# Kernel tuning notes

Measured on AMD Instinct MI355X. Metric: run time of the kernel, lower is better.

## Reference

```python
import jax, jax.numpy as jnp
import numpy as np

B, L, DM = 4, 4096, 1024
DK, DV = 128, 128


def setup_inputs() -> dict:
    key = jax.random.key(0)
    kq, kk, kv, kwq, kwk, kwv = jax.random.split(key, 6)
    scale = 1.0 / np.sqrt(DM)
    return {
        "Q": jax.random.normal(kq, (B, L, DM), dtype=jnp.float32),
        "K": jax.random.normal(kk, (B, L, DM), dtype=jnp.float32),
        "V": jax.random.normal(kv, (B, L, DM), dtype=jnp.float32),
        "mask": jnp.ones((B, 1, L), dtype=jnp.int32),
        "WQ": jax.random.normal(kwq, (DM, DK), dtype=jnp.float32) * scale,
        "WK": jax.random.normal(kwk, (DM, DK), dtype=jnp.float32) * scale,
        "WV": jax.random.normal(kwv, (DM, DV), dtype=jnp.float32) * scale,
    }


def reference(Q, K, V, mask, WQ, WK, WV):
    # Projections (Dense, no bias): [B, L, dm] @ [dm, dk/dv]
    q = jnp.einsum("bld,dk->blk", Q, WQ)  # [B, L, dk]
    k = jnp.einsum("bld,dk->blk", K, WK)  # [B, L, dk]
    v = jnp.einsum("bld,dv->blv", V, WV)  # [B, L, dv]
    # Raw scores [B, L, L]
    qk = jnp.einsum("bqk,bsk->bqs", q, k)
    # Faithful to original: mask applied BEFORE scaling by 1/sqrt(dk)
    qk = jnp.where(mask == 1, qk, -jnp.inf)
    qk = qk / jnp.sqrt(jnp.asarray(DK, dtype=qk.dtype))
    attn = jax.nn.softmax(qk, axis=-1)
    return jnp.einsum("bqs,bsv->bqv", attn, v)  # [B, L, dv]
```

## Files before the change

### kernel.cpp

```cpp
#include <hip/hip_runtime.h>
#include <hip/hip_bf16.h>

#define B_  4
#define L_  4096
#define DM_ 1024
#define DK_ 128
#define DV_ 128
#define KS_ 4
#define ROWS_ (B_ * L_)

typedef __bf16 bf16x8 __attribute__((ext_vector_type(8)));
typedef float  f32x4  __attribute__((ext_vector_type(4)));

__device__ __forceinline__ float wred_max16(float v) {
    v = fmaxf(v, __shfl_xor(v, 1, 64));
    v = fmaxf(v, __shfl_xor(v, 2, 64));
    v = fmaxf(v, __shfl_xor(v, 4, 64));
    v = fmaxf(v, __shfl_xor(v, 8, 64));
    return v;
}
__device__ __forceinline__ float wred_sum16(float v) {
    v += __shfl_xor(v, 1, 64);
    v += __shfl_xor(v, 2, 64);
    v += __shfl_xor(v, 4, 64);
    v += __shfl_xor(v, 8, 64);
    return v;
}

__global__ __launch_bounds__(256) void wt_kernel(
    const float* __restrict__ WQ, const float* __restrict__ WK,
    const float* __restrict__ WV, __bf16* __restrict__ WT)
{
    const int mat = blockIdx.y;
    const float* W = (mat == 0) ? WQ : (mat == 1) ? WK : WV;
    __bf16* Wt = WT + (size_t)mat * DK_ * DM_;

    __shared__ float lds[DK_][33];
    const int t  = threadIdx.x;
    const int d0 = blockIdx.x * 32;

    for (int i = 0; i < 16; ++i) {
        int idx = i * 256 + t;
        int dd = idx >> 7, n = idx & 127;
        lds[n][dd] = W[(size_t)(d0 + dd) * DK_ + n];
    }
    __syncthreads();
    for (int i = 0; i < 16; ++i) {
        int idx = i * 256 + t;
        int n = idx >> 5, dd = idx & 31;
        Wt[(size_t)n * DM_ + d0 + dd] = (__bf16)lds[n][dd];
    }
}

__global__ __launch_bounds__(256) void proj_kernel(
    const float* __restrict__ Q, const float* __restrict__ K, const float* __restrict__ V,
    const __bf16* __restrict__ WT,
    __bf16* __restrict__ qb, __bf16* __restrict__ kb, __bf16* __restrict__ vT)
{
    const int mat = blockIdx.y;
    const float* X = (mat == 0) ? Q : (mat == 1) ? K : V;
    const __bf16* Wt = WT + (size_t)mat * DK_ * DM_;

    __shared__ __bf16 w_lds[128][132];

    const int t    = threadIdx.x;
    const int w    = t >> 6;
    const int l    = t & 63;
    const int quad = l >> 4;
    const int c16  = l & 15;
    const int m0   = blockIdx.x * 64 + w * 16;
    const float* xrow = &X[(size_t)(m0 + c16) * DM_];

    f32x4 acc[8];
    for (int i = 0; i < 8; ++i) acc[i] = {0.f, 0.f, 0.f, 0.f};

    for (int kt8 = 0; kt8 < 8; ++kt8) {
        const int d0 = kt8 * 128;
        __syncthreads();
        for (int i = 0; i < 8; ++i) {
            int e = i * 256 + t;
            int n = e >> 4, blk = e & 15;
            *(int4*)&w_lds[n][blk * 8] = *(const int4*)&Wt[(size_t)n * DM_ + d0 + blk * 8];
        }
        __syncthreads();

        for (int dd = 0; dd < 4; ++dd) {
            const float* xp = xrow + d0 + dd * 32 + quad * 8;
            float4 x0 = *(const float4*)xp;
            float4 x1 = *(const float4*)(xp + 4);
            bf16x8 af;
            af[0] = (__bf16)x0.x; af[1] = (__bf16)x0.y; af[2] = (__bf16)x0.z; af[3] = (__bf16)x0.w;
            af[4] = (__bf16)x1.x; af[5] = (__bf16)x1.y; af[6] = (__bf16)x1.z; af[7] = (__bf16)x1.w;
            for (int nt = 0; nt < 8; ++nt) {
                bf16x8 bfv = *(const bf16x8*)&w_lds[nt * 16 + c16][dd * 32 + quad * 8];
                acc[nt] = __builtin_amdgcn_mfma_f32_16x16x32_bf16(af, bfv, acc[nt], 0, 0, 0);
            }
        }
    }

    if (mat < 2) {
        __bf16* outp = (mat == 0) ? qb : kb;
        for (int nt = 0; nt < 8; ++nt)
            for (int r = 0; r < 4; ++r)
                outp[(size_t)(m0 + quad * 4 + r) * DK_ + nt * 16 + c16] = (__bf16)acc[nt][r];
    } else {
        for (int nt = 0; nt < 8; ++nt)
            for (int r = 0; r < 4; ++r) {
                int row = m0 + quad * 4 + r;
                int b = row >> 12, s = row & (L_ - 1);
                vT[((size_t)b * DV_ + nt * 16 + c16) * L_ + s] = (__bf16)acc[nt][r];
            }
    }
}

__global__ __launch_bounds__(256) void attn_kernel(
    const __bf16* __restrict__ qb, const __bf16* __restrict__ kb,
    const __bf16* __restrict__ vT, const int* __restrict__ mask,
    __bf16* __restrict__ ob_part, float* __restrict__ ml_part)
{
    __shared__ __bf16 k_lds[64][140];
    __shared__ __bf16 v_lds[128][76];
    __shared__ __bf16 p_lds[4][16][76];

    const int t    = threadIdx.x;
    const int w    = t >> 6;
    const int l    = t & 63;
    const int quad = l >> 4;
    const int c16  = l & 15;

    const int combo = blockIdx.x & 15;
    const int b     = combo & 3;
    const int ks    = combo >> 2;
    const int qt    = blockIdx.x >> 4;
    const int m0    = qt * 64 + w * 16;
    const size_t bL = (size_t)b * L_;
    const int kbase = ks * (L_ / KS_);

    bf16x8 qf[4];
    {
        const __bf16* qrow = &qb[(bL + m0 + c16) * DK_];
        for (int dt = 0; dt < 4; ++dt)
            qf[dt] = *(const bf16x8*)&qrow[dt * 32 + quad * 8];
    }

    f32x4 o[8];
    for (int i = 0; i < 8; ++i) o[i] = {0.f, 0.f, 0.f, 0.f};
    float mst[4], lst[4];
    for (int r = 0; r < 4; ++r) { mst[r] = -1e30f; lst[r] = 0.f; }

    const float sm_scale = 0.088388347648318447f;

    for (int sc = 0; sc < (L_ / KS_) / 64; ++sc) {
        const int s0 = kbase + sc * 64;
        __syncthreads();
        for (int i = 0; i < 4; ++i) {
            int e = i * 256 + t;
            int kr = e >> 4, c8 = (e & 15) << 3;
            *(int4*)&k_lds[kr][c8] = *(const int4*)&kb[(bL + s0 + kr) * DK_ + c8];
        }
        for (int i = 0; i < 4; ++i) {
            int e = i * 256 + t;
            int vr = e >> 3, s8 = (e & 7) << 3;
            *(int4*)&v_lds[vr][s8] = *(const int4*)&vT[((size_t)b * DV_ + vr) * L_ + s0 + s8];
        }
        __syncthreads();

        f32x4 sacc[4];
        for (int nt = 0; nt < 4; ++nt) sacc[nt] = {0.f, 0.f, 0.f, 0.f};
        for (int dt = 0; dt < 4; ++dt)
            for (int nt = 0; nt < 4; ++nt) {
                bf16x8 kf = *(const bf16x8*)&k_lds[nt * 16 + c16][dt * 32 + quad * 8];
                sacc[nt] = __builtin_amdgcn_mfma_f32_16x16x32_bf16(qf[dt], kf, sacc[nt], 0, 0, 0);
            }

        int mk[4];
        for (int nt = 0; nt < 4; ++nt) mk[nt] = mask[bL + s0 + nt * 16 + c16];
        for (int nt = 0; nt < 4; ++nt)
            for (int r = 0; r < 4; ++r) {
                float s = sacc[nt][r] * sm_scale;
                sacc[nt][r] = (mk[nt] == 1) ? s : -1e30f;
            }

        float alpha[4];
        for (int r = 0; r < 4; ++r) {
            float cm = fmaxf(fmaxf(sacc[0][r], sacc[1][r]), fmaxf(sacc[2][r], sacc[3][r]));
            cm = wred_max16(cm);
            float nm = fmaxf(mst[r], cm);
            alpha[r] = __expf(mst[r] - nm);
            float psum = 0.f;
            for (int nt = 0; nt < 4; ++nt) {
                float p = __expf(sacc[nt][r] - nm);
                __bf16 pbv = (__bf16)p;
                p_lds[w][quad * 4 + r][nt * 16 + c16] = pbv;
                psum += (float)pbv;
            }
            psum = wred_sum16(psum);
            lst[r] = lst[r] * alpha[r] + psum;
            mst[r] = nm;
        }
        __asm__ volatile("s_waitcnt lgkmcnt(0)" ::: "memory");

        for (int vt = 0; vt < 8; ++vt)
            for (int r = 0; r < 4; ++r)
                o[vt][r] *= alpha[r];

        for (int kt = 0; kt < 2; ++kt) {
            bf16x8 pf = *(const bf16x8*)&p_lds[w][c16][kt * 32 + quad * 8];
            for (int vt = 0; vt < 8; ++vt) {
                bf16x8 vf = *(const bf16x8*)&v_lds[vt * 16 + c16][kt * 32 + quad * 8];
                o[vt] = __builtin_amdgcn_mfma_f32_16x16x32_bf16(pf, vf, o[vt], 0, 0, 0);
            }
        }
    }

    __bf16* op = ob_part + ((size_t)ks * ROWS_ + bL + m0) * DV_;
    for (int vt = 0; vt < 8; ++vt)
        for (int r = 0; r < 4; ++r)
            op[(size_t)(quad * 4 + r) * DV_ + vt * 16 + c16] = (__bf16)o[vt][r];
    if (c16 == 0)
        for (int r = 0; r < 4; ++r) {
            size_t row = (size_t)ks * ROWS_ + bL + m0 + quad * 4 + r;
            ml_part[row * 2 + 0] = mst[r];
            ml_part[row * 2 + 1] = lst[r];
        }
}

__global__ __launch_bounds__(256) void combine_kernel(
    const __bf16* __restrict__ ob_part, const float* __restrict__ ml_part,
    float* __restrict__ out)
{
    const int gid = blockIdx.x * 256 + threadIdx.x;
    const int row = gid >> 5;
    const int c4  = (gid & 31) << 2;

    float m[KS_], lv[KS_];
    float M = -1e30f;
    for (int s = 0; s < KS_; ++s) {
        m[s]  = ml_part[((size_t)s * ROWS_ + row) * 2 + 0];
        lv[s] = ml_part[((size_t)s * ROWS_ + row) * 2 + 1];
        M = fmaxf(M, m[s]);
    }
    float Lt = 0.f, acc[4] = {0.f, 0.f, 0.f, 0.f};
    for (int s = 0; s < KS_; ++s) {
        float ws = __expf(m[s] - M);
        Lt += lv[s] * ws;
        const __bf16* op = ob_part + ((size_t)s * ROWS_ + row) * DV_ + c4;
        for (int c = 0; c < 4; ++c) acc[c] += (float)op[c] * ws;
    }
    float rL = 1.0f / Lt;
    for (int c = 0; c < 4; ++c)
        out[(size_t)row * DV_ + c4 + c] = acc[c] * rL;
}

extern "C" void kernel_launch(void* const* d_in, const int* in_sizes, int n_in,
                              void* d_out, int out_size, void* d_ws, size_t ws_size,
                              hipStream_t stream) {
    const float* Q    = (const float*)d_in[0];
    const float* K    = (const float*)d_in[1];
    const float* V    = (const float*)d_in[2];
    const int*   mask = (const int*)d_in[3];
    const float* WQ   = (const float*)d_in[4];
    const float* WK   = (const float*)d_in[5];
    const float* WV   = (const float*)d_in[6];
    float* out = (float*)d_out;

    __bf16* qb = (__bf16*)d_ws;
    __bf16* kb = qb + (size_t)ROWS_ * DK_;
    __bf16* vT = kb + (size_t)ROWS_ * DK_;
    __bf16* WT = vT + (size_t)ROWS_ * DV_;
    __bf16* ob_part = WT + (size_t)3 * DK_ * DM_;
    float*  ml_part = (float*)(ob_part + (size_t)KS_ * ROWS_ * DV_);

    wt_kernel<<<dim3(DM_ / 32, 3), 256, 0, stream>>>(WQ, WK, WV, WT);
    proj_kernel<<<dim3(ROWS_ / 64, 3), 256, 0, stream>>>(Q, K, V, WT, qb, kb, vT);
    attn_kernel<<<dim3((ROWS_ / 64) * KS_), 256, 0, stream>>>(qb, kb, vT, mask, ob_part, ml_part);
    combine_kernel<<<dim3(ROWS_ * 32 / 256), 256, 0, stream>>>(ob_part, ml_part, out);
}
```

Before: 335.0 us.

## Prefetch tiles via registers, fold scale into WQ, use MFMA row sums and DPP reductions

Projection and attention kernels now preload the next weight/K/V tile into registers while the current tile is consumed, replacing plain syncthreads with waitcnt+barrier. The softmax scale is folded into the WQ transpose, mask checks are precomputed into a per-chunk bitmask so all-ones chunks skip masking, row max uses DPP instead of shuffles, rescaling is skipped when no row max grows, and row sums come from an extra MFMA against a ones vector. These aim to hide global load latency and cut VALU/shuffle work in the softmax loop, at the cost of more registers and one extra MFMA per step.

```diff
diff --git a/kernel.cpp b/kernel.cpp
--- a/kernel.cpp
+++ b/kernel.cpp
@@ -12,18 +12,18 @@
 typedef __bf16 bf16x8 __attribute__((ext_vector_type(8)));
 typedef float  f32x4  __attribute__((ext_vector_type(4)));
 
-__device__ __forceinline__ float wred_max16(float v) {
-    v = fmaxf(v, __shfl_xor(v, 1, 64));
-    v = fmaxf(v, __shfl_xor(v, 2, 64));
-    v = fmaxf(v, __shfl_xor(v, 4, 64));
-    v = fmaxf(v, __shfl_xor(v, 8, 64));
-    return v;
-}
-__device__ __forceinline__ float wred_sum16(float v) {
-    v += __shfl_xor(v, 1, 64);
-    v += __shfl_xor(v, 2, 64);
-    v += __shfl_xor(v, 4, 64);
-    v += __shfl_xor(v, 8, 64);
+#define BAR_LGKM() __asm__ volatile("s_waitcnt lgkmcnt(0)\ns_barrier" ::: "memory")
+
+__device__ __forceinline__ float rowmax_dpp(float v) {
+    int x;
+    x = __float_as_int(v);
+    v = fmaxf(v, __int_as_float(__builtin_amdgcn_update_dpp(x, x, 0x121, 0xF, 0xF, false)));
+    x = __float_as_int(v);
+    v = fmaxf(v, __int_as_float(__builtin_amdgcn_update_dpp(x, x, 0x122, 0xF, 0xF, false)));
+    x = __float_as_int(v);
+    v = fmaxf(v, __int_as_float(__builtin_amdgcn_update_dpp(x, x, 0x124, 0xF, 0xF, false)));
+    x = __float_as_int(v);
+    v = fmaxf(v, __int_as_float(__builtin_amdgcn_update_dpp(x, x, 0x128, 0xF, 0xF, false)));
     return v;
 }
 
@@ -33,6 +33,7 @@
 {
     const int mat = blockIdx.y;
     const float* W = (mat == 0) ? WQ : (mat == 1) ? WK : WV;
+    const float scl = (mat == 0) ? 0.088388347648318447f : 1.0f;
     __bf16* Wt = WT + (size_t)mat * DK_ * DM_;
 
     __shared__ float lds[DK_][33];
@@ -42,7 +43,7 @@
     for (int i = 0; i < 16; ++i) {
         int idx = i * 256 + t;
         int dd = idx >> 7, n = idx & 127;
-        lds[n][dd] = W[(size_t)(d0 + dd) * DK_ + n];
+        lds[n][dd] = W[(size_t)(d0 + dd) * DK_ + n] * scl;
     }
     __syncthreads();
     for (int i = 0; i < 16; ++i) {
@@ -71,18 +72,25 @@
     const int m0   = blockIdx.x * 64 + w * 16;
     const float* xrow = &X[(size_t)(m0 + c16) * DM_];
 
+    const int sn  = t >> 4;
+    const int sb8 = (t & 15) << 3;
+
     f32x4 acc[8];
     for (int i = 0; i < 8; ++i) acc[i] = {0.f, 0.f, 0.f, 0.f};
 
+    int4 wreg[8];
+    for (int i = 0; i < 8; ++i)
+        wreg[i] = *(const int4*)&Wt[(size_t)(i * 16 + sn) * DM_ + sb8];
+
     for (int kt8 = 0; kt8 < 8; ++kt8) {
         const int d0 = kt8 * 128;
-        __syncthreads();
-        for (int i = 0; i < 8; ++i) {
-            int e = i * 256 + t;
-            int n = e >> 4, blk = e & 15;
-            *(int4*)&w_lds[n][blk * 8] = *(const int4*)&Wt[(size_t)n * DM_ + d0 + blk * 8];
-        }
-        __syncthreads();
+        BAR_LGKM();
+        for (int i = 0; i < 8; ++i)
+            *(int4*)&w_lds[i * 16 + sn][sb8] = wreg[i];
+        if (kt8 < 7)
+            for (int i = 0; i < 8; ++i)
+                wreg[i] = *(const int4*)&Wt[(size_t)(i * 16 + sn) * DM_ + d0 + 128 + sb8];
+        BAR_LGKM();
 
         for (int dd = 0; dd < 4; ++dd) {
             const float* xp = xrow + d0 + dd * 32 + quad * 8;
@@ -136,6 +144,9 @@
     const size_t bL = (size_t)b * L_;
     const int kbase = ks * (L_ / KS_);
 
+    const int skr = t >> 4, skc = (t & 15) << 3;
+    const int svr = t >> 3, svc = (t & 7) << 3;
+
     bf16x8 qf[4];
     {
         const __bf16* qrow = &qb[(bL + m0 + c16) * DK_];
@@ -143,27 +154,48 @@
             qf[dt] = *(const bf16x8*)&qrow[dt * 32 + quad * 8];
     }
 
-    f32x4 o[8];
+    unsigned int mbits = 0;
+    for (int sc = 0; sc < 16; ++sc) {
+        int mv = mask[bL + kbase + sc * 64 + l];
+        mbits |= (unsigned int)(__ballot(mv == 1) == ~0ull) << sc;
+    }
+
+    bf16x8 onesv;
+    for (int i = 0; i < 8; ++i) onesv[i] = (__bf16)1.0f;
+
+    f32x4 o[8], osum;
     for (int i = 0; i < 8; ++i) o[i] = {0.f, 0.f, 0.f, 0.f};
-    float mst[4], lst[4];
-    for (int r = 0; r < 4; ++r) { mst[r] = -1e30f; lst[r] = 0.f; }
-
-    const float sm_scale = 0.088388347648318447f;
+    osum = {0.f, 0.f, 0.f, 0.f};
+    float mst[4];
+    for (int r = 0; r < 4; ++r) mst[r] = -1e30f;
+
+    int4 kreg[4], vreg[4];
+    {
+        const __bf16* kp = &kb[(bL + kbase + skr) * DK_ + skc];
+        for (int i = 0; i < 4; ++i)
+            kreg[i] = *(const int4*)&kp[(size_t)i * 16 * DK_];
+        const __bf16* vp = &vT[((size_t)b * DV_ + svr) * L_ + kbase + svc];
+        for (int i = 0; i < 4; ++i)
+            vreg[i] = *(const int4*)&vp[(size_t)i * 32 * L_];
+    }
 
     for (int sc = 0; sc < (L_ / KS_) / 64; ++sc) {
         const int s0 = kbase + sc * 64;
-        __syncthreads();
-        for (int i = 0; i < 4; ++i) {
-            int e = i * 256 + t;
-            int kr = e >> 4, c8 = (e & 15) << 3;
-            *(int4*)&k_lds[kr][c8] = *(const int4*)&kb[(bL + s0 + kr) * DK_ + c8];
-        }
-        for (int i = 0; i < 4; ++i) {
-            int e = i * 256 + t;
-            int vr = e >> 3, s8 = (e & 7) << 3;
-            *(int4*)&v_lds[vr][s8] = *(const int4*)&vT[((size_t)b * DV_ + vr) * L_ + s0 + s8];
-        }
-        __syncthreads();
+
+        BAR_LGKM();
+        for (int i = 0; i < 4; ++i)
+            *(int4*)&k_lds[i * 16 + skr][skc] = kreg[i];
+        for (int i = 0; i < 4; ++i)
+            *(int4*)&v_lds[i * 32 + svr][svc] = vreg[i];
+        if (sc < 15) {
+            const __bf16* kp = &kb[(bL + s0 + 64 + skr) * DK_ + skc];
+            for (int i = 0; i < 4; ++i)
+                kreg[i] = *(const int4*)&kp[(size_t)i * 16 * DK_];
+            const __bf16* vp = &vT[((size_t)b * DV_ + svr) * L_ + s0 + 64 + svc];
+            for (int i = 0; i < 4; ++i)
+                vreg[i] = *(const int4*)&vp[(size_t)i * 32 * L_];
+        }
+        BAR_LGKM();
 
         f32x4 sacc[4];
         for (int nt = 0; nt < 4; ++nt) sacc[nt] = {0.f, 0.f, 0.f, 0.f};
@@ -173,36 +205,39 @@
                 sacc[nt] = __builtin_amdgcn_mfma_f32_16x16x32_bf16(qf[dt], kf, sacc[nt], 0, 0, 0);
             }
 
-        int mk[4];
-        for (int nt = 0; nt < 4; ++nt) mk[nt] = mask[bL + s0 + nt * 16 + c16];
-        for (int nt = 0; nt < 4; ++nt)
-            for (int r = 0; r < 4; ++r) {
-                float s = sacc[nt][r] * sm_scale;
-                sacc[nt][r] = (mk[nt] == 1) ? s : -1e30f;
-            }
-
-        float alpha[4];
+        if (!((mbits >> sc) & 1)) {
+            for (int nt = 0; nt < 4; ++nt) {
+                int mk = mask[bL + s0 + nt * 16 + c16];
+                for (int r = 0; r < 4; ++r)
+                    if (mk != 1) sacc[nt][r] = -1e30f;
+            }
+        }
+
+        float nm[4];
+        bool up = false;
         for (int r = 0; r < 4; ++r) {
             float cm = fmaxf(fmaxf(sacc[0][r], sacc[1][r]), fmaxf(sacc[2][r], sacc[3][r]));
-            cm = wred_max16(cm);
-            float nm = fmaxf(mst[r], cm);
-            alpha[r] = __expf(mst[r] - nm);
-            float psum = 0.f;
+            cm = rowmax_dpp(cm);
+            nm[r] = fmaxf(mst[r], cm);
+            up |= (nm[r] > mst[r]);
+        }
+        if (__ballot(up)) {
+            float alpha[4];
+            for (int r = 0; r < 4; ++r) {
+                alpha[r] = __expf(mst[r] - nm[r]);
+                mst[r] = nm[r];
+            }
+            for (int vt = 0; vt < 8; ++vt)
+                for (int r = 0; r < 4; ++r) o[vt][r] *= alpha[r];
+            for (int r = 0; r < 4; ++r) osum[r] *= alpha[r];
+        }
+
+        for (int r = 0; r < 4; ++r)
             for (int nt = 0; nt < 4; ++nt) {
-                float p = __expf(sacc[nt][r] - nm);
-                __bf16 pbv = (__bf16)p;
-                p_lds[w][quad * 4 + r][nt * 16 + c16] = pbv;
-                psum += (float)pbv;
-            }
-            psum = wred_sum16(psum);
-            lst[r] = lst[r] * alpha[r] + psum;
-            mst[r] = nm;
-        }
+                float p = __expf(sacc[nt][r] - nm[r]);
+                p_lds[w][quad * 4 + r][nt * 16 + c16] = (__bf16)p;
+            }
         __asm__ volatile("s_waitcnt lgkmcnt(0)" ::: "memory");
-
-        for (int vt = 0; vt < 8; ++vt)
-            for (int r = 0; r < 4; ++r)
-                o[vt][r] *= alpha[r];
 
         for (int kt = 0; kt < 2; ++kt) {
             bf16x8 pf = *(const bf16x8*)&p_lds[w][c16][kt * 32 + quad * 8];
@@ -210,6 +245,7 @@
                 bf16x8 vf = *(const bf16x8*)&v_lds[vt * 16 + c16][kt * 32 + quad * 8];
                 o[vt] = __builtin_amdgcn_mfma_f32_16x16x32_bf16(pf, vf, o[vt], 0, 0, 0);
             }
+            osum = __builtin_amdgcn_mfma_f32_16x16x32_bf16(pf, onesv, osum, 0, 0, 0);
         }
     }
 
@@ -221,7 +257,7 @@
         for (int r = 0; r < 4; ++r) {
             size_t row = (size_t)ks * ROWS_ + bL + m0 + quad * 4 + r;
             ml_part[row * 2 + 0] = mst[r];
-            ml_part[row * 2 + 1] = lst[r];
+            ml_part[row * 2 + 1] = osum[r];
         }
 }
 
```

Measured after the change: 466.6 us. 39.3% more time.
